# Kernel optimization log

Measured on AMD Instinct MI355X. Metric: run time of the kernel, lower is better.

The kernel has to match this reference:

```python
import jax, jax.numpy as jnp
import numpy as np

N, K, D = 20000, 32, 128  # nodes, neighbors per node, key_dim


def setup_inputs() -> dict:
    key = jax.random.key(0)
    ks = jax.random.split(key, 7)
    s = 1.0 / np.sqrt(D).astype(np.float32)
    return {
        "middle_key": jax.random.normal(ks[0], (N, K, D), jnp.float32),
        "nodes_key": jax.random.normal(ks[1], (N, D), jnp.float32),
        "middle_value": jax.random.normal(ks[2], (N, K, D), jnp.float32),
        "W1": jax.random.normal(ks[3], (D, D), jnp.float32) * s,  # attention_weight1.weight
        "W2": jax.random.normal(ks[4], (D, D), jnp.float32) * s,  # attention_weight2.weight
        "a_w": jax.random.normal(ks[5], (D,), jnp.float32) * s,   # a_weight.weight (row vector)
        "a_b": jax.random.normal(ks[6], (1,), jnp.float32),        # a_weight.bias
    }


def reference(middle_key, nodes_key, middle_value, W1, W2, a_w, a_b):
    # nn.Linear computes x @ W.T
    p1 = nodes_key @ W1.T                                  # [N, D] (center-node projection)
    p2 = jnp.einsum('nkd,ed->nke', middle_key, W2)          # [N, K, D] (neighbor projection)
    # a_weight(...) then tanh -> scalar score per neighbor
    scores = jnp.tanh(
        jnp.einsum('nke,e->nk', p1[:, None, :] + p2, a_w) + a_b[0]
    )                                                       # [N, K]
    # softmax over neighbor axis (dim=-2 of the [N, K, 1] tensor in torch)
    coef = jax.nn.softmax(scores, axis=-1)[..., None]       # [N, K, 1]
    # weighted sum over neighbors
    return jnp.sum(coef * middle_value, axis=-2)            # [N, D]
```

## Files before the change

### kernel.cpp

```cpp
#include <hip/hip_runtime.h>
#include <hip/hip_bf16.h>

#define NN 20000
#define KK 32
#define DD 128

__global__ __launch_bounds__(DD) void fold_weights_kernel(
    const float* __restrict__ W1, const float* __restrict__ W2,
    const float* __restrict__ a_w, const float* __restrict__ a_b,
    float* __restrict__ ws) {
  const int d = threadIdx.x;
  float s1 = 0.f, s2 = 0.f;
#pragma unroll 8
  for (int e = 0; e < DD; ++e) {
    const float aw = a_w[e];
    s1 += aw * W1[e * DD + d];
    s2 += aw * W2[e * DD + d];
  }
  ws[d] = s1;
  ws[DD + d] = s2;
  if (d == 0) ws[2 * DD] = a_b[0];
}

__global__ __launch_bounds__(256) void attn_agg_kernel(
    const float* __restrict__ mk, const float* __restrict__ nk,
    const float* __restrict__ mv, const float* __restrict__ ws,
    float* __restrict__ out) {
  const int n = blockIdx.x;
  const int t = threadIdx.x;
  const int f = t & 31;
  const int kg = t >> 5;

  __shared__ float s_scores[KK];
  __shared__ float s_coef[KK];
  __shared__ float s_center;
  __shared__ float4 s_part[4][32];

  const float4* v2p = (const float4*)(ws + DD);
  const float4 w2 = v2p[f];

  if (t < 32) {
    const float4 a = ((const float4*)(nk + (size_t)n * DD))[t];
    const float4 b = ((const float4*)ws)[t];
    float c = a.x * b.x + a.y * b.y + a.z * b.z + a.w * b.w;
#pragma unroll
    for (int o = 16; o >= 1; o >>= 1) c += __shfl_xor(c, o, 64);
    if (t == 0) s_center = c;
  }

  const float4* mkp = (const float4*)(mk + (size_t)n * KK * DD);
  float dj[4];
#pragma unroll
  for (int j = 0; j < 4; ++j) {
    const int k = kg + 8 * j;
    const float4 a = mkp[k * (DD / 4) + f];
    dj[j] = a.x * w2.x + a.y * w2.y + a.z * w2.z + a.w * w2.w;
  }
#pragma unroll
  for (int j = 0; j < 4; ++j) {
    float v = dj[j];
#pragma unroll
    for (int o = 16; o >= 1; o >>= 1) v += __shfl_xor(v, o, 64);
    if (f == 0) s_scores[kg + 8 * j] = v;
  }
  __syncthreads();

  if (t < 32) {
    const float b = ws[2 * DD];
    const float s = tanhf(s_scores[t] + s_center + b);
    const float e = expf(s);
    float sum = e;
#pragma unroll
    for (int o = 16; o >= 1; o >>= 1) sum += __shfl_xor(sum, o, 64);
    s_coef[t] = e / sum;
  }
  __syncthreads();

  const float4* mvp = (const float4*)(mv + (size_t)n * KK * DD);
  float4 acc = make_float4(0.f, 0.f, 0.f, 0.f);
#pragma unroll
  for (int j = 0; j < 4; ++j) {
    const int k = kg + 8 * j;
    const float c = s_coef[k];
    const float4 v = mvp[k * (DD / 4) + f];
    acc.x += c * v.x;
    acc.y += c * v.y;
    acc.z += c * v.z;
    acc.w += c * v.w;
  }
  acc.x += __shfl_xor(acc.x, 32, 64);
  acc.y += __shfl_xor(acc.y, 32, 64);
  acc.z += __shfl_xor(acc.z, 32, 64);
  acc.w += __shfl_xor(acc.w, 32, 64);

  const int w = t >> 6;
  if ((t & 63) < 32) s_part[w][f] = acc;
  __syncthreads();

  if (t < 32) {
    float4 r = s_part[0][t];
    const float4 r1 = s_part[1][t];
    const float4 r2 = s_part[2][t];
    const float4 r3 = s_part[3][t];
    r.x += r1.x + r2.x + r3.x;
    r.y += r1.y + r2.y + r3.y;
    r.z += r1.z + r2.z + r3.z;
    r.w += r1.w + r2.w + r3.w;
    ((float4*)(out + (size_t)n * DD))[t] = r;
  }
}

extern "C" void kernel_launch(void* const* d_in, const int* in_sizes, int n_in,
                              void* d_out, int out_size, void* d_ws, size_t ws_size,
                              hipStream_t stream) {
  const float* middle_key = (const float*)d_in[0];
  const float* nodes_key = (const float*)d_in[1];
  const float* middle_value = (const float*)d_in[2];
  const float* W1 = (const float*)d_in[3];
  const float* W2 = (const float*)d_in[4];
  const float* a_w = (const float*)d_in[5];
  const float* a_b = (const float*)d_in[6];
  float* out = (float*)d_out;
  float* ws = (float*)d_ws;

  fold_weights_kernel<<<1, DD, 0, stream>>>(W1, W2, a_w, a_b, ws);
  attn_agg_kernel<<<NN, 256, 0, stream>>>(middle_key, nodes_key, middle_value,
                                          ws, out);
}
```

Baseline: 129.0 us.

## Prefetch keys and values together, compute softmax redundantly per warp, drop a barrier

Loads both middle_key and middle_value tiles into registers up front with nontemporal loads, so the value stream overlaps the score computation instead of starting after the softmax. Every 32-lane group now computes the softmax itself and fetches coefficients with shuffles, which removes the s_coef shared array and one __syncthreads. The output uses a nontemporal store. Register use rises because eight float4s are held live per thread, and the tanh/exp work is repeated in every group.

```diff
diff --git a/kernel.cpp b/kernel.cpp
--- a/kernel.cpp
+++ b/kernel.cpp
@@ -4,6 +4,8 @@
 #define NN 20000
 #define KK 32
 #define DD 128
+
+typedef float f4 __attribute__((ext_vector_type(4)));
 
 __global__ __launch_bounds__(DD) void fold_weights_kernel(
     const float* __restrict__ W1, const float* __restrict__ W2,
@@ -32,81 +34,69 @@
   const int kg = t >> 5;
 
   __shared__ float s_scores[KK];
-  __shared__ float s_coef[KK];
   __shared__ float s_center;
-  __shared__ float4 s_part[4][32];
+  __shared__ f4 s_part[4][32];
 
-  const float4* v2p = (const float4*)(ws + DD);
-  const float4 w2 = v2p[f];
+  const f4* mkp = (const f4*)(mk + (size_t)n * KK * DD);
+  const f4* mvp = (const f4*)(mv + (size_t)n * KK * DD);
+
+  f4 ak[4], av[4];
+#pragma unroll
+  for (int j = 0; j < 4; ++j) {
+    const int k = kg + 8 * j;
+    ak[j] = __builtin_nontemporal_load(mkp + k * (DD / 4) + f);
+    av[j] = __builtin_nontemporal_load(mvp + k * (DD / 4) + f);
+  }
+
+  const f4 w2 = ((const f4*)(ws + DD))[f];
 
   if (t < 32) {
-    const float4 a = ((const float4*)(nk + (size_t)n * DD))[t];
-    const float4 b = ((const float4*)ws)[t];
-    float c = a.x * b.x + a.y * b.y + a.z * b.z + a.w * b.w;
+    const f4 a = __builtin_nontemporal_load((const f4*)(nk + (size_t)n * DD) + t);
+    const f4 b = ((const f4*)ws)[t];
+    const f4 m = a * b;
+    float c = m[0] + m[1] + m[2] + m[3];
 #pragma unroll
     for (int o = 16; o >= 1; o >>= 1) c += __shfl_xor(c, o, 64);
     if (t == 0) s_center = c;
   }
 
-  const float4* mkp = (const float4*)(mk + (size_t)n * KK * DD);
-  float dj[4];
 #pragma unroll
   for (int j = 0; j < 4; ++j) {
-    const int k = kg + 8 * j;
-    const float4 a = mkp[k * (DD / 4) + f];
-    dj[j] = a.x * w2.x + a.y * w2.y + a.z * w2.z + a.w * w2.w;
-  }
-#pragma unroll
-  for (int j = 0; j < 4; ++j) {
-    float v = dj[j];
+    const f4 m = ak[j] * w2;
+    float v = m[0] + m[1] + m[2] + m[3];
 #pragma unroll
     for (int o = 16; o >= 1; o >>= 1) v += __shfl_xor(v, o, 64);
     if (f == 0) s_scores[kg + 8 * j] = v;
   }
   __syncthreads();
 
-  if (t < 32) {
-    const float b = ws[2 * DD];
-    const float s = tanhf(s_scores[t] + s_center + b);
-    const float e = expf(s);
-    float sum = e;
+  const float bias = ws[2 * DD];
+  const float ctr = s_center;
+  const float sc = tanhf(s_scores[f] + ctr + bias);
+  const float e = expf(sc);
+  float sum = e;
 #pragma unroll
-    for (int o = 16; o >= 1; o >>= 1) sum += __shfl_xor(sum, o, 64);
-    s_coef[t] = e / sum;
-  }
-  __syncthreads();
+  for (int o = 16; o >= 1; o >>= 1) sum += __shfl_xor(sum, o, 64);
+  const float inv = 1.f / sum;
 
-  const float4* mvp = (const float4*)(mv + (size_t)n * KK * DD);
-  float4 acc = make_float4(0.f, 0.f, 0.f, 0.f);
+  f4 acc = {0.f, 0.f, 0.f, 0.f};
 #pragma unroll
   for (int j = 0; j < 4; ++j) {
-    const int k = kg + 8 * j;
-    const float c = s_coef[k];
-    const float4 v = mvp[k * (DD / 4) + f];
-    acc.x += c * v.x;
-    acc.y += c * v.y;
-    acc.z += c * v.z;
-    acc.w += c * v.w;
+    const float cj = __shfl(e, kg + 8 * j, 64) * inv;
+    acc += cj * av[j];
   }
-  acc.x += __shfl_xor(acc.x, 32, 64);
-  acc.y += __shfl_xor(acc.y, 32, 64);
-  acc.z += __shfl_xor(acc.z, 32, 64);
-  acc.w += __shfl_xor(acc.w, 32, 64);
+  acc[0] += __shfl_xor(acc[0], 32, 64);
+  acc[1] += __shfl_xor(acc[1], 32, 64);
+  acc[2] += __shfl_xor(acc[2], 32, 64);
+  acc[3] += __shfl_xor(acc[3], 32, 64);
 
   const int w = t >> 6;
   if ((t & 63) < 32) s_part[w][f] = acc;
   __syncthreads();
 
   if (t < 32) {
-    float4 r = s_part[0][t];
-    const float4 r1 = s_part[1][t];
-    const float4 r2 = s_part[2][t];
-    const float4 r3 = s_part[3][t];
-    r.x += r1.x + r2.x + r3.x;
-    r.y += r1.y + r2.y + r3.y;
-    r.z += r1.z + r2.z + r3.z;
-    r.w += r1.w + r2.w + r3.w;
-    ((float4*)(out + (size_t)n * DD))[t] = r;
+    const f4 r = s_part[0][t] + s_part[1][t] + s_part[2][t] + s_part[3][t];
+    __builtin_nontemporal_store(r, (f4*)(out + (size_t)n * DD) + t);
   }
 }
 
```

Measured after the change: 110.1 us. 1.17x faster.
